# Kernel tuning notes

Hardware: AMD Instinct MI355X
Metric: run time of the kernel (lower is better)

The kernel has to match this reference:

```python
import jax, jax.numpy as jnp
import numpy as np

# Model dims (match init_kwargs)
U, I, E = 100000, 50000, 1000000   # users, items, interactions
FD, EK, EF = 64, 64, 64            # feature_dim, embed_k, embed_f
L = 3                              # n_layers
B = 16384                          # scoring batch
ALPHA = [1.0 / (k + 1) for k in range(L + 1)]


def setup_inputs() -> dict:
    key = jax.random.key(0)
    ks = jax.random.split(key, 9)
    Gu = jax.random.normal(ks[0], (U, EK), jnp.float32) * 0.05
    Gi = jax.random.normal(ks[1], (I, EK), jnp.float32) * 0.05
    F = jax.random.normal(ks[2], (FD, EF), jnp.float32) * 0.1
    proj_w = jax.random.normal(ks[3], (EF, 1), jnp.float32) * 0.1
    proj_b = jnp.zeros((1,), jnp.float32)
    # sparse binary-ish decomposition-path feature matrix (dense here)
    edge_features = (jax.random.uniform(ks[4], (E, FD)) < 0.1).astype(jnp.float32)
    u = jax.random.randint(ks[5], (E,), 0, U)
    it = jax.random.randint(ks[6], (E,), 0, I) + U  # items offset by num_users
    edge_index = jnp.stack([jnp.concatenate([u, it]),
                            jnp.concatenate([it, u])]).astype(jnp.int64)  # [2, 2E]
    users = jax.random.randint(ks[7], (B,), 0, U).astype(jnp.int64)
    items = jax.random.randint(ks[8], (B,), 0, I).astype(jnp.int64)
    return dict(Gu=Gu, Gi=Gi, F=F, proj_w=proj_w, proj_b=proj_b,
                edge_features=edge_features, edge_index=edge_index,
                users=users, items=items)


def _propagate(Gu, Gi, F, proj_w, proj_b, edge_features, edge_index):
    N = U + I
    src, dst = edge_index[0], edge_index[1]
    # edge-feature projection -> scalar edge weight, duplicated per direction
    ew = (edge_features @ F) @ proj_w + proj_b            # [E, 1]
    ew = jnp.concatenate([ew, ew], axis=0)[:, 0]          # [2E]
    # symmetric GCN normalization over the bipartite interaction graph
    deg = jax.ops.segment_sum(jnp.ones_like(ew), dst, num_segments=N)  # [N]
    dinv = jnp.where(deg > 0, jax.lax.rsqrt(jnp.maximum(deg, 1.0)), 0.0)
    coef = (dinv[src] * dinv[dst] * ew)[:, None]          # [2E, 1]
    x = jnp.concatenate([Gu, Gi], axis=0)                 # [N, K]
    out = ALPHA[0] * x
    for k in range(L):  # edge-conditioned gather -> scale -> scatter-add
        x = jax.ops.segment_sum(coef * x[src], dst, num_segments=N)
        out = out + ALPHA[k + 1] * x
    return out[:U], out[U:]


def reference(Gu, Gi, F, proj_w, proj_b, edge_features, edge_index, users, items):
    gu, gi = _propagate(Gu, Gi, F, proj_w, proj_b, edge_features, edge_index)
    # forward(): masked dot-product scoring of (user, item) pairs
    return jnp.sum(gu[users] * gi[items], axis=1)  # [B]
```

## Files before the change

### kernel.cpp

```cpp
#include <hip/hip_runtime.h>

constexpr int Uc = 100000;
constexpr int Ic = 50000;
constexpr int Nc = 150000;
constexpr int Ec = 1000000;
constexpr int Bc = 16384;
constexpr int NBS = (Nc + 1023) / 1024;


__global__ void k_fproj(const float* __restrict__ F, const float* __restrict__ pw,
                        float* __restrict__ Fp) {
    int d = threadIdx.x;
    if (d < 64) {
        float s = 0.f;
#pragma unroll
        for (int j = 0; j < 64; ++j) s += F[d * 64 + j] * pw[j];
        Fp[d] = s;
    }
}

__global__ void k_deg2(const int* __restrict__ un, const int* __restrict__ in_,
                       unsigned* __restrict__ deg) {
    int e = blockIdx.x * blockDim.x + threadIdx.x;
    if (e < Ec) {
        atomicAdd(&deg[un[e]], 1u);
        atomicAdd(&deg[in_[e]], 1u);
    }
}

__global__ void k_scan1(const unsigned* __restrict__ deg, int* __restrict__ rowptr,
                        int* __restrict__ bsums, float* __restrict__ dinv) {
    __shared__ int sh[256];
    int tid = threadIdx.x, bid = blockIdx.x;
    int base = bid * 1024 + tid * 4;
    int v0 = (base + 0 < Nc) ? (int)deg[base + 0] : 0;
    int v1 = (base + 1 < Nc) ? (int)deg[base + 1] : 0;
    int v2 = (base + 2 < Nc) ? (int)deg[base + 2] : 0;
    int v3 = (base + 3 < Nc) ? (int)deg[base + 3] : 0;
    if (base + 0 < Nc) dinv[base + 0] = v0 ? rsqrtf((float)v0) : 0.f;
    if (base + 1 < Nc) dinv[base + 1] = v1 ? rsqrtf((float)v1) : 0.f;
    if (base + 2 < Nc) dinv[base + 2] = v2 ? rsqrtf((float)v2) : 0.f;
    if (base + 3 < Nc) dinv[base + 3] = v3 ? rsqrtf((float)v3) : 0.f;
    int s = v0 + v1 + v2 + v3;
    sh[tid] = s;
    __syncthreads();
    for (int off = 1; off < 256; off <<= 1) {
        int t = (tid >= off) ? sh[tid - off] : 0;
        __syncthreads();
        sh[tid] += t;
        __syncthreads();
    }
    int excl = sh[tid] - s;
    if (tid == 255) bsums[bid] = sh[255];
    if (base + 0 < Nc) rowptr[base + 0] = excl;
    if (base + 1 < Nc) rowptr[base + 1] = excl + v0;
    if (base + 2 < Nc) rowptr[base + 2] = excl + v0 + v1;
    if (base + 3 < Nc) rowptr[base + 3] = excl + v0 + v1 + v2;
}

__global__ void k_scan2(int* __restrict__ bsums, int nb) {
    __shared__ int sh[256];
    int tid = threadIdx.x;
    int v = (tid < nb) ? bsums[tid] : 0;
    sh[tid] = v;
    __syncthreads();
    for (int off = 1; off < 256; off <<= 1) {
        int t = (tid >= off) ? sh[tid - off] : 0;
        __syncthreads();
        sh[tid] += t;
        __syncthreads();
    }
    if (tid < nb) bsums[tid] = sh[tid] - v;
}

__global__ void k_scan3(int* __restrict__ rowptr, const int* __restrict__ bsums,
                        int* __restrict__ cursor) {
    int i = blockIdx.x * blockDim.x + threadIdx.x;
    if (i < Nc) {
        int r = rowptr[i] + bsums[i >> 10];
        rowptr[i] = r;
        cursor[i] = r;
    }
    if (i == 0) rowptr[Nc] = 2 * Ec;
}

__global__ void k_build(const int* __restrict__ un, const int* __restrict__ in_,
                        const float* __restrict__ ef, const float* __restrict__ Fp,
                        const float* __restrict__ pb, const float* __restrict__ dinv,
                        int* __restrict__ cursor, int2* __restrict__ csr) {
    int t = blockIdx.x * blockDim.x + threadIdx.x;
    int e = t >> 4, l = t & 15;
    if (e >= Ec) return;
    float4 f = reinterpret_cast<const float4*>(ef)[(size_t)e * 16 + l];
    float4 w = reinterpret_cast<const float4*>(Fp)[l];
    float s = f.x * w.x + f.y * w.y + f.z * w.z + f.w * w.w;
    s += __shfl_xor(s, 8, 16);
    s += __shfl_xor(s, 4, 16);
    s += __shfl_xor(s, 2, 16);
    s += __shfl_xor(s, 1, 16);
    if (l == 0 || l == 8) {
        int uu = un[e], ii = in_[e];
        float c = dinv[uu] * dinv[ii] * (s + pb[0]);
        if (l == 0) {
            int pos = atomicAdd(&cursor[ii], 1);
            csr[pos] = make_int2(uu, __float_as_int(c));
        } else {
            int pos = atomicAdd(&cursor[uu], 1);
            csr[pos] = make_int2(ii, __float_as_int(c));
        }
    }
}

template <int SPLIT>
__global__ void k_gprop(const int* __restrict__ rowptr, const int2* __restrict__ csr,
                        const float* __restrict__ xGu, const float* __restrict__ xGi,
                        float* __restrict__ xn) {
    int t = blockIdx.x * blockDim.x + threadIdx.x;
    int n = t >> 4, l = t & 15;
    if (n >= Nc) return;
    int e0 = rowptr[n], e1 = rowptr[n + 1];
    const float4* xs;
    int off = 0;
    if (SPLIT) {
        if (n < Uc) { xs = reinterpret_cast<const float4*>(xGi); off = Uc * 16; }
        else        { xs = reinterpret_cast<const float4*>(xGu); }
    } else {
        xs = reinterpret_cast<const float4*>(xGu);
    }
    float4 acc = make_float4(0.f, 0.f, 0.f, 0.f);
    int e = e0;
    for (; e + 4 <= e1; e += 4) {
        int2 s0 = csr[e], s1 = csr[e + 1], s2 = csr[e + 2], s3 = csr[e + 3];
        float4 v0 = xs[s0.x * 16 - off + l];
        float4 v1 = xs[s1.x * 16 - off + l];
        float4 v2 = xs[s2.x * 16 - off + l];
        float4 v3 = xs[s3.x * 16 - off + l];
        float c0 = __int_as_float(s0.y), c1 = __int_as_float(s1.y);
        float c2 = __int_as_float(s2.y), c3 = __int_as_float(s3.y);
        acc.x += c0 * v0.x + c1 * v1.x + c2 * v2.x + c3 * v3.x;
        acc.y += c0 * v0.y + c1 * v1.y + c2 * v2.y + c3 * v3.y;
        acc.z += c0 * v0.z + c1 * v1.z + c2 * v2.z + c3 * v3.z;
        acc.w += c0 * v0.w + c1 * v1.w + c2 * v2.w + c3 * v3.w;
    }
    for (; e < e1; ++e) {
        int2 sc = csr[e];
        float c = __int_as_float(sc.y);
        float4 v = xs[sc.x * 16 - off + l];
        acc.x += c * v.x; acc.y += c * v.y; acc.z += c * v.z; acc.w += c * v.w;
    }
    reinterpret_cast<float4*>(xn)[n * 16 + l] = acc;
}

__global__ void k_final(const float* __restrict__ Gu, const float* __restrict__ Gi,
                        const float* __restrict__ x1, const float* __restrict__ x2,
                        const int* __restrict__ rowptr, const int2* __restrict__ csr,
                        const int* __restrict__ users, const int* __restrict__ items,
                        float* __restrict__ out) {
    int wid = (blockIdx.x * blockDim.x + threadIdx.x) >> 6;
    int d = threadIdx.x & 63;
    if (wid >= Bc) return;
    int un = users[wid];
    int in_ = Uc + items[wid];

    float acc2[2];
#pragma unroll
    for (int side = 0; side < 2; ++side) {
        int n = side ? in_ : un;
        float base = side ? Gi[(size_t)(n - Uc) * 64 + d] : Gu[(size_t)n * 64 + d];
        float a = base + 0.5f * x1[(size_t)n * 64 + d] + (1.f / 3.f) * x2[(size_t)n * 64 + d];
        float su = 0.f;
        int e0 = rowptr[n], e1 = rowptr[n + 1];
        int e = e0;
        for (; e + 4 <= e1; e += 4) {
            int2 s0 = csr[e], s1 = csr[e + 1], s2 = csr[e + 2], s3 = csr[e + 3];
            float v0 = x2[(size_t)s0.x * 64 + d];
            float v1 = x2[(size_t)s1.x * 64 + d];
            float v2 = x2[(size_t)s2.x * 64 + d];
            float v3 = x2[(size_t)s3.x * 64 + d];
            su += __int_as_float(s0.y) * v0 + __int_as_float(s1.y) * v1 +
                  __int_as_float(s2.y) * v2 + __int_as_float(s3.y) * v3;
        }
        for (; e < e1; ++e) {
            int2 sc = csr[e];
            su += __int_as_float(sc.y) * x2[(size_t)sc.x * 64 + d];
        }
        acc2[side] = a + 0.25f * su;
    }

    float p = acc2[0] * acc2[1];
#pragma unroll
    for (int o = 32; o > 0; o >>= 1) p += __shfl_xor(p, o, 64);
    if (d == 0) out[wid] = p;
}


extern "C" void kernel_launch(void* const* d_in, const int* in_sizes, int n_in,
                              void* d_out, int out_size, void* d_ws, size_t ws_size,
                              hipStream_t stream) {
    const float* Gu = (const float*)d_in[0];
    const float* Gi = (const float*)d_in[1];
    const float* F  = (const float*)d_in[2];
    const float* pw = (const float*)d_in[3];
    const float* pb = (const float*)d_in[4];
    const float* ef = (const float*)d_in[5];
    const int*   ei = (const int*)d_in[6];
    const int* users = (const int*)d_in[7];
    const int* items = (const int*)d_in[8];
    float* out = (float*)d_out;

    float* ws = (float*)d_ws;
    float*    Fp     = ws;
    float*    dinv   = Fp + 64;
    unsigned* deg    = (unsigned*)(dinv + Nc);
    int*      rowptr = (int*)(deg + Nc);
    int*      cursor = rowptr + (Nc + 16);
    int*      bsums  = cursor + Nc;
    int2*     csr    = (int2*)(bsums + 256);
    float*    xa     = (float*)(csr + 2 * Ec);
    float*    xb     = xa + (size_t)Nc * 64;

    const int* un  = ei;
    const int* in_ = ei + 2 * Ec;

    hipMemsetAsync(deg, 0, Nc * sizeof(unsigned), stream);
    k_fproj<<<1, 64, 0, stream>>>(F, pw, Fp);
    k_deg2<<<(Ec + 255) / 256, 256, 0, stream>>>(un, in_, deg);
    k_scan1<<<NBS, 256, 0, stream>>>(deg, rowptr, bsums, dinv);
    k_scan2<<<1, 256, 0, stream>>>(bsums, NBS);
    k_scan3<<<(Nc + 255) / 256, 256, 0, stream>>>(rowptr, bsums, cursor);
    k_build<<<(Ec * 16) / 256, 256, 0, stream>>>(un, in_, ef, Fp, pb, dinv, cursor, csr);

    k_gprop<1><<<(Nc * 16 + 255) / 256, 256, 0, stream>>>(rowptr, csr, Gu, Gi, xa);
    k_gprop<0><<<(Nc * 16 + 255) / 256, 256, 0, stream>>>(rowptr, csr, xa, nullptr, xb);

    k_final<<<(Bc * 64) / 256, 256, 0, stream>>>(Gu, Gi, xa, xb, rowptr, csr, users, items, out);
}
```

Measured before the change: 403.1 us.

## Fuse small setup kernels, unroll gathers by eight with nontemporal CSR loads

Merges the feature projection into the degree-count kernel, and folds the block-sum scan into the rowptr fixup kernel, with each block redoing the small scan in shared memory. This removes two launches. The gather loops in propagation and final scoring now read CSR entries as 64-bit nontemporal loads and are unrolled by eight for more memory-level parallelism. The propagation block size also drops to 128. The costs are more register pressure and redundant per-block scan work.

Measured after the change: 423.5 us. +5.1%, slower.

```diff
diff --git a/kernel.cpp b/kernel.cpp
--- a/kernel.cpp
+++ b/kernel.cpp
@@ -8,19 +8,17 @@
 constexpr int NBS = (Nc + 1023) / 1024;
 
 
-__global__ void k_fproj(const float* __restrict__ F, const float* __restrict__ pw,
-                        float* __restrict__ Fp) {
-    int d = threadIdx.x;
-    if (d < 64) {
+__global__ void k_deg2_fproj(const int* __restrict__ un, const int* __restrict__ in_,
+                             unsigned* __restrict__ deg,
+                             const float* __restrict__ F, const float* __restrict__ pw,
+                             float* __restrict__ Fp) {
+    if (blockIdx.x == 0 && threadIdx.x < 64) {
+        int d = threadIdx.x;
         float s = 0.f;
 #pragma unroll
         for (int j = 0; j < 64; ++j) s += F[d * 64 + j] * pw[j];
         Fp[d] = s;
     }
-}
-
-__global__ void k_deg2(const int* __restrict__ un, const int* __restrict__ in_,
-                       unsigned* __restrict__ deg) {
     int e = blockIdx.x * blockDim.x + threadIdx.x;
     if (e < Ec) {
         atomicAdd(&deg[un[e]], 1u);
@@ -58,10 +56,11 @@
     if (base + 3 < Nc) rowptr[base + 3] = excl + v0 + v1 + v2;
 }
 
-__global__ void k_scan2(int* __restrict__ bsums, int nb) {
+__global__ void k_scan3(int* __restrict__ rowptr, const int* __restrict__ bsums,
+                        int* __restrict__ cursor) {
     __shared__ int sh[256];
     int tid = threadIdx.x;
-    int v = (tid < nb) ? bsums[tid] : 0;
+    int v = (tid < NBS) ? bsums[tid] : 0;
     sh[tid] = v;
     __syncthreads();
     for (int off = 1; off < 256; off <<= 1) {
@@ -70,14 +69,13 @@
         sh[tid] += t;
         __syncthreads();
     }
-    if (tid < nb) bsums[tid] = sh[tid] - v;
-}
-
-__global__ void k_scan3(int* __restrict__ rowptr, const int* __restrict__ bsums,
-                        int* __restrict__ cursor) {
+    int excl = sh[tid] - v;
+    __syncthreads();
+    sh[tid] = excl;
+    __syncthreads();
     int i = blockIdx.x * blockDim.x + threadIdx.x;
     if (i < Nc) {
-        int r = rowptr[i] + bsums[i >> 10];
+        int r = rowptr[i] + sh[i >> 10];
         rowptr[i] = r;
         cursor[i] = r;
     }
@@ -112,7 +110,7 @@
 }
 
 template <int SPLIT>
-__global__ void k_gprop(const int* __restrict__ rowptr, const int2* __restrict__ csr,
+__global__ void k_gprop(const int* __restrict__ rowptr, const long long* __restrict__ csr,
                         const float* __restrict__ xGu, const float* __restrict__ xGi,
                         float* __restrict__ xn) {
     int t = blockIdx.x * blockDim.x + threadIdx.x;
@@ -129,23 +127,40 @@
     }
     float4 acc = make_float4(0.f, 0.f, 0.f, 0.f);
     int e = e0;
-    for (; e + 4 <= e1; e += 4) {
-        int2 s0 = csr[e], s1 = csr[e + 1], s2 = csr[e + 2], s3 = csr[e + 3];
-        float4 v0 = xs[s0.x * 16 - off + l];
-        float4 v1 = xs[s1.x * 16 - off + l];
-        float4 v2 = xs[s2.x * 16 - off + l];
-        float4 v3 = xs[s3.x * 16 - off + l];
-        float c0 = __int_as_float(s0.y), c1 = __int_as_float(s1.y);
-        float c2 = __int_as_float(s2.y), c3 = __int_as_float(s3.y);
-        acc.x += c0 * v0.x + c1 * v1.x + c2 * v2.x + c3 * v3.x;
-        acc.y += c0 * v0.y + c1 * v1.y + c2 * v2.y + c3 * v3.y;
-        acc.z += c0 * v0.z + c1 * v1.z + c2 * v2.z + c3 * v3.z;
-        acc.w += c0 * v0.w + c1 * v1.w + c2 * v2.w + c3 * v3.w;
+    for (; e + 8 <= e1; e += 8) {
+        long long q0 = __builtin_nontemporal_load(csr + e + 0);
+        long long q1 = __builtin_nontemporal_load(csr + e + 1);
+        long long q2 = __builtin_nontemporal_load(csr + e + 2);
+        long long q3 = __builtin_nontemporal_load(csr + e + 3);
+        long long q4 = __builtin_nontemporal_load(csr + e + 4);
+        long long q5 = __builtin_nontemporal_load(csr + e + 5);
+        long long q6 = __builtin_nontemporal_load(csr + e + 6);
+        long long q7 = __builtin_nontemporal_load(csr + e + 7);
+        float4 v0 = xs[(int)q0 * 16 - off + l];
+        float4 v1 = xs[(int)q1 * 16 - off + l];
+        float4 v2 = xs[(int)q2 * 16 - off + l];
+        float4 v3 = xs[(int)q3 * 16 - off + l];
+        float4 v4 = xs[(int)q4 * 16 - off + l];
+        float4 v5 = xs[(int)q5 * 16 - off + l];
+        float4 v6 = xs[(int)q6 * 16 - off + l];
+        float4 v7 = xs[(int)q7 * 16 - off + l];
+        float c0 = __int_as_float((int)(q0 >> 32)), c1 = __int_as_float((int)(q1 >> 32));
+        float c2 = __int_as_float((int)(q2 >> 32)), c3 = __int_as_float((int)(q3 >> 32));
+        float c4 = __int_as_float((int)(q4 >> 32)), c5 = __int_as_float((int)(q5 >> 32));
+        float c6 = __int_as_float((int)(q6 >> 32)), c7 = __int_as_float((int)(q7 >> 32));
+        acc.x += c0 * v0.x + c1 * v1.x + c2 * v2.x + c3 * v3.x
+               + c4 * v4.x + c5 * v5.x + c6 * v6.x + c7 * v7.x;
+        acc.y += c0 * v0.y + c1 * v1.y + c2 * v2.y + c3 * v3.y
+               + c4 * v4.y + c5 * v5.y + c6 * v6.y + c7 * v7.y;
+        acc.z += c0 * v0.z + c1 * v1.z + c2 * v2.z + c3 * v3.z
+               + c4 * v4.z + c5 * v5.z + c6 * v6.z + c7 * v7.z;
+        acc.w += c0 * v0.w + c1 * v1.w + c2 * v2.w + c3 * v3.w
+               + c4 * v4.w + c5 * v5.w + c6 * v6.w + c7 * v7.w;
     }
     for (; e < e1; ++e) {
-        int2 sc = csr[e];
-        float c = __int_as_float(sc.y);
-        float4 v = xs[sc.x * 16 - off + l];
+        long long q = __builtin_nontemporal_load(csr + e);
+        float c = __int_as_float((int)(q >> 32));
+        float4 v = xs[(int)q * 16 - off + l];
         acc.x += c * v.x; acc.y += c * v.y; acc.z += c * v.z; acc.w += c * v.w;
     }
     reinterpret_cast<float4*>(xn)[n * 16 + l] = acc;
@@ -153,7 +168,7 @@
 
 __global__ void k_final(const float* __restrict__ Gu, const float* __restrict__ Gi,
                         const float* __restrict__ x1, const float* __restrict__ x2,
-                        const int* __restrict__ rowptr, const int2* __restrict__ csr,
+                        const int* __restrict__ rowptr, const long long* __restrict__ csr,
                         const int* __restrict__ users, const int* __restrict__ items,
                         float* __restrict__ out) {
     int wid = (blockIdx.x * blockDim.x + threadIdx.x) >> 6;
@@ -171,18 +186,27 @@
         float su = 0.f;
         int e0 = rowptr[n], e1 = rowptr[n + 1];
         int e = e0;
-        for (; e + 4 <= e1; e += 4) {
-            int2 s0 = csr[e], s1 = csr[e + 1], s2 = csr[e + 2], s3 = csr[e + 3];
-            float v0 = x2[(size_t)s0.x * 64 + d];
-            float v1 = x2[(size_t)s1.x * 64 + d];
-            float v2 = x2[(size_t)s2.x * 64 + d];
-            float v3 = x2[(size_t)s3.x * 64 + d];
-            su += __int_as_float(s0.y) * v0 + __int_as_float(s1.y) * v1 +
-                  __int_as_float(s2.y) * v2 + __int_as_float(s3.y) * v3;
+        for (; e + 8 <= e1; e += 8) {
+            long long q0 = __builtin_nontemporal_load(csr + e + 0);
+            long long q1 = __builtin_nontemporal_load(csr + e + 1);
+            long long q2 = __builtin_nontemporal_load(csr + e + 2);
+            long long q3 = __builtin_nontemporal_load(csr + e + 3);
+            long long q4 = __builtin_nontemporal_load(csr + e + 4);
+            long long q5 = __builtin_nontemporal_load(csr + e + 5);
+            long long q6 = __builtin_nontemporal_load(csr + e + 6);
+            long long q7 = __builtin_nontemporal_load(csr + e + 7);
+            su += __int_as_float((int)(q0 >> 32)) * x2[(size_t)(int)q0 * 64 + d]
+                + __int_as_float((int)(q1 >> 32)) * x2[(size_t)(int)q1 * 64 + d]
+                + __int_as_float((int)(q2 >> 32)) * x2[(size_t)(int)q2 * 64 + d]
+                + __int_as_float((int)(q3 >> 32)) * x2[(size_t)(int)q3 * 64 + d]
+                + __int_as_float((int)(q4 >> 32)) * x2[(size_t)(int)q4 * 64 + d]
+                + __int_as_float((int)(q5 >> 32)) * x2[(size_t)(int)q5 * 64 + d]
+                + __int_as_float((int)(q6 >> 32)) * x2[(size_t)(int)q6 * 64 + d]
+                + __int_as_float((int)(q7 >> 32)) * x2[(size_t)(int)q7 * 64 + d];
         }
         for (; e < e1; ++e) {
-            int2 sc = csr[e];
-            su += __int_as_float(sc.y) * x2[(size_t)sc.x * 64 + d];
+            long long q = __builtin_nontemporal_load(csr + e);
+            su += __int_as_float((int)(q >> 32)) * x2[(size_t)(int)q * 64 + d];
         }
         acc2[side] = a + 0.25f * su;
     }
@@ -223,15 +247,13 @@
     const int* in_ = ei + 2 * Ec;
 
     hipMemsetAsync(deg, 0, Nc * sizeof(unsigned), stream);
-    k_fproj<<<1, 64, 0, stream>>>(F, pw, Fp);
-    k_deg2<<<(Ec + 255) / 256, 256, 0, stream>>>(un, in_, deg);
+    k_deg2_fproj<<<(Ec + 255) / 256, 256, 0, stream>>>(un, in_, deg, F, pw, Fp);
     k_scan1<<<NBS, 256, 0, stream>>>(deg, rowptr, bsums, dinv);
-    k_scan2<<<1, 256, 0, stream>>>(bsums, NBS);
     k_scan3<<<(Nc + 255) / 256, 256, 0, stream>>>(rowptr, bsums, cursor);
     k_build<<<(Ec * 16) / 256, 256, 0, stream>>>(un, in_, ef, Fp, pb, dinv, cursor, csr);
 
-    k_gprop<1><<<(Nc * 16 + 255) / 256, 256, 0, stream>>>(rowptr, csr, Gu, Gi, xa);
-    k_gprop<0><<<(Nc * 16 + 255) / 256, 256, 0, stream>>>(rowptr, csr, xa, nullptr, xb);
-
-    k_final<<<(Bc * 64) / 256, 256, 0, stream>>>(Gu, Gi, xa, xb, rowptr, csr, users, items, out);
-}
+    k_gprop<1><<<(Nc * 16 + 127) / 128, 128, 0, stream>>>(rowptr, (const long long*)csr, Gu, Gi, xa);
+    k_gprop<0><<<(Nc * 16 + 127) / 128, 128, 0, stream>>>(rowptr, (const long long*)csr, xa, nullptr, xb);
+
+    k_final<<<(Bc * 64) / 256, 256, 0, stream>>>(Gu, Gi, xa, xb, rowptr, (const long long*)csr, users, items, out);
+}
```
